# Optimization experiments

Measured on AMD Instinct MI355X. Metric: run time of the kernel, lower is better.

The kernel has to match this reference:

```python
import jax, jax.numpy as jnp
from jax import lax
import numpy as np

B, R, NOBJ, SIZE = 16, 64, 32, 64  # batch, rels/image, objs/image, map size


def setup_inputs() -> dict:
    key = jax.random.key(0)
    ks = jax.random.split(key, 8)
    # boxes as (x1, y1, x2, y2) in an arbitrary image coordinate frame
    xy1 = jax.random.uniform(ks[0], (B, NOBJ, 2), dtype=jnp.float32) * 80.0
    wh = jax.random.uniform(ks[1], (B, NOBJ, 2), dtype=jnp.float32) * 40.0 + 2.0
    bboxes = jnp.concatenate([xy1, xy1 + wh], axis=-1)  # [B, NOBJ, 4]
    num_obj = jnp.full((B,), NOBJ, dtype=jnp.int32)
    num_relation = jnp.full((B,), R, dtype=jnp.int32)  # constant -> static tot_num_rels
    object_pairs = jax.random.randint(ks[2], (B, R, 2), 0, NOBJ)
    conv1_w = jax.random.normal(ks[3], (64, 2, 5, 5), dtype=jnp.float32) * 0.1
    conv1_b = jnp.zeros((64,), dtype=jnp.float32)
    conv2_w = jax.random.normal(ks[4], (32, 64, 5, 5), dtype=jnp.float32) * 0.05
    conv2_b = jnp.zeros((32,), dtype=jnp.float32)
    fc_w = jax.random.normal(ks[5], (512, 32), dtype=jnp.float32) * 0.1
    fc_b = jnp.zeros((512,), dtype=jnp.float32)
    return dict(bboxes=bboxes, num_obj=num_obj, num_relation=num_relation,
                object_pairs=object_pairs, conv1_w=conv1_w, conv1_b=conv1_b,
                conv2_w=conv2_w, conv2_b=conv2_b, fc_w=fc_w, fc_b=fc_b)


def _sp_maps(bboxes, object_pairs):
    # Vectorized replacement of the per-relation python loop + get_sp:
    # both boxes of a pair are rescaled into the 64x64 frame of their union
    # box and rasterized as binary masks (iCAN-style 2-channel spatial config).
    Bc, Rc, _ = object_pairs.shape
    pairs = object_pairs.reshape(-1, 2)                      # [T, 2]
    b_idx = jnp.repeat(jnp.arange(Bc), Rc)                   # [T]
    b0 = bboxes[b_idx, pairs[:, 0]]                          # [T, 4]
    b1 = bboxes[b_idx, pairs[:, 1]]                          # [T, 4]
    ux1 = jnp.minimum(b0[:, 0], b1[:, 0])
    uy1 = jnp.minimum(b0[:, 1], b1[:, 1])
    ux2 = jnp.maximum(b0[:, 2], b1[:, 2])
    uy2 = jnp.maximum(b0[:, 3], b1[:, 3])
    uw = jnp.maximum(ux2 - ux1, 1e-6)
    uh = jnp.maximum(uy2 - uy1, 1e-6)

    def scale(b):  # union-normalized box in [0, SIZE] grid coords
        return jnp.stack([(b[:, 0] - ux1) / uw * SIZE,
                          (b[:, 1] - uy1) / uh * SIZE,
                          (b[:, 2] - ux1) / uw * SIZE,
                          (b[:, 3] - uy1) / uh * SIZE], axis=-1)

    coords = jnp.arange(SIZE, dtype=jnp.float32) + 0.5
    gx = coords[None, None, :]   # [1, 1, SIZE]
    gy = coords[None, :, None]   # [1, SIZE, 1]

    def rasterize(sb):  # sb: [T, 4] -> [T, SIZE, SIZE]
        x1 = sb[:, 0, None, None]; y1 = sb[:, 1, None, None]
        x2 = sb[:, 2, None, None]; y2 = sb[:, 3, None, None]
        return ((gx >= x1) & (gx <= x2) & (gy >= y1) & (gy <= y2)).astype(jnp.float32)

    return jnp.stack([rasterize(scale(b0)), rasterize(scale(b1))], axis=1)  # [T,2,64,64]


def _conv(x, w, b):
    y = lax.conv_general_dilated(x, w, window_strides=(1, 1), padding='VALID',
                                 dimension_numbers=('NCHW', 'OIHW', 'NCHW'))
    return y + b[None, :, None, None]


def _maxpool2(x):
    return lax.reduce_window(x, -jnp.inf, lax.max, (1, 1, 2, 2), (1, 1, 2, 2), 'VALID')


def reference(bboxes, num_obj, num_relation, object_pairs,
              conv1_w, conv1_b, conv2_w, conv2_b, fc_w, fc_b):
    sp = _sp_maps(bboxes, object_pairs)        # [T, 2, 64, 64]
    x = _maxpool2(_conv(sp, conv1_w, conv1_b)) # [T, 64, 30, 30]
    x = _maxpool2(_conv(x, conv2_w, conv2_b))  # [T, 32, 13, 13]
    x = jnp.mean(x, axis=(2, 3))               # AvgPool((13,13)) -> [T, 32]
    return jax.nn.relu(x @ fc_w.T + fc_b)      # [T, 512]
```

## Files before the change

kernel.cpp:

```cpp
#include <hip/hip_runtime.h>
#include <stdint.h>

typedef unsigned long long u64;
typedef short v8s __attribute__((ext_vector_type(8)));
typedef float v4f __attribute__((ext_vector_type(4)));

__device__ __forceinline__ unsigned short f2bf_rne(float f) {
  union { float f; unsigned u; } c; c.f = f;
  unsigned u = c.u;
  u += 0x7fffu + ((u >> 16) & 1u);
  return (unsigned short)(u >> 16);
}

__global__ __launch_bounds__(256) void prepack_w2(
    const float* __restrict__ w2, unsigned short* __restrict__ Wr) {
  int idx = blockIdx.x * 256 + threadIdx.x;
  if (idx >= 32 * 1600) return;
  int c = idx / 1600, rem = idx - c * 1600;
  int h = rem / 800, r2 = rem - h * 800;
  int tap = r2 >> 5, chh = r2 & 31;
  Wr[h * 25600 + c * 800 + r2] = f2bf_rne(w2[(c * 64 + h * 32 + chh) * 25 + tap]);
}

__global__ __launch_bounds__(512, 4) void fused_kernel(
    const float* __restrict__ bboxes,
    const int*   __restrict__ pairs,
    const float* __restrict__ w1,
    const float* __restrict__ b1,
    const unsigned short* __restrict__ Wr,
    const float* __restrict__ b2,
    const float* __restrict__ fcw,
    const float* __restrict__ fcb,
    float* __restrict__ out)
{
  extern __shared__ char smem[];
  unsigned short* Xs = (unsigned short*)smem;
  float* P8      = (float*)(smem + 61200);
  float* Cout    = (float*)smem;
  float* partial = (float*)(smem + 61200);
  float* fs      = (float*)(smem + 61200 + 1024);

  const int n = blockIdx.x, t = threadIdx.x;
  const int lane = t & 63, wv = t >> 6;
  const int q = lane >> 4, ln = lane & 15;

  const int bb = n >> 6, rr_ = n & 63;
  const int p0 = pairs[(bb * 64 + rr_) * 2 + 0];
  const int p1 = pairs[(bb * 64 + rr_) * 2 + 1];
  const float* A  = bboxes + (bb * 32 + p0) * 4;
  const float* Bq = bboxes + (bb * 32 + p1) * 4;
  const float ax1 = A[0],  ay1 = A[1],  ax2 = A[2],  ay2 = A[3];
  const float cx1 = Bq[0], cy1 = Bq[1], cx2 = Bq[2], cy2 = Bq[3];
  const float ux1 = fminf(ax1, cx1), uy1 = fminf(ay1, cy1);
  const float ux2 = fmaxf(ax2, cx2), uy2 = fmaxf(ay2, cy2);
  const float uw = fmaxf(ux2 - ux1, 1e-6f), uh = fmaxf(uy2 - uy1, 1e-6f);
  const float g = (float)lane + 0.5f;
  u64 ixs[2], iys[2];
  {
    float X1 = (ax1 - ux1) / uw * 64.f, X2 = (ax2 - ux1) / uw * 64.f;
    float Y1 = (ay1 - uy1) / uh * 64.f, Y2 = (ay2 - uy1) / uh * 64.f;
    ixs[0] = __ballot(g >= X1 && g <= X2);
    iys[0] = __ballot(g >= Y1 && g <= Y2);
  }
  {
    float X1 = (cx1 - ux1) / uw * 64.f, X2 = (cx2 - ux1) / uw * 64.f;
    float Y1 = (cy1 - uy1) / uh * 64.f, Y2 = (cy2 - uy1) / uh * 64.f;
    ixs[1] = __ballot(g >= X1 && g <= X2);
    iys[1] = __ballot(g >= Y1 && g <= Y2);
  }

  v4f acc[6][2];
  int pclamp[6], baseB[6];
  int cnt = 0;
  #pragma unroll
  for (int it = 0; it < 6; it++) {
    int nt = wv + it * 8;
    if (nt < 43) {
      int p = nt * 16 + ln; if (p > 675) p = 675;
      pclamp[it] = p;
      int y = p / 26, x = p - y * 26;
      baseB[it] = (y * 30 + x) * 68 + q * 16;
      cnt = it + 1;
    } else { pclamp[it] = 0; baseB[it] = 0; }
    acc[it][0] = (v4f)0.f; acc[it][1] = (v4f)0.f;
  }

  for (int h = 0; h < 2; h++) {
    for (int c8 = 0; c8 < 4; c8++) {
      const int cbase = h * 32 + c8 * 8;
      for (int e = t; e < 960; e += 512) {
        int cidx = e / 120, rem = e - cidx * 120;
        int ch = rem / 60, x = rem - ch * 60;
        unsigned bits = (unsigned)(ixs[ch] >> x) & 31u;
        const float* wr = w1 + (cbase + cidx) * 50 + ch * 25;
        float* Pp = P8 + cidx * 610 + ch * 305 + x;
        float p = 0.f;
        #pragma unroll
        for (int i = 0; i < 5; i++) {
          float rcv = 0.f;
          #pragma unroll
          for (int j = 0; j < 5; j++)
            rcv += ((bits >> j) & 1u) ? wr[i * 5 + j] : 0.f;
          p += rcv;
          Pp[i * 61] = p;
        }
      }
      __syncthreads();
      float b1v[8];
      #pragma unroll
      for (int i = 0; i < 8; i++) b1v[i] = b1[cbase + i];
      for (int pix = t; pix < 900; pix += 512) {
        int qy = pix / 30, qx = pix - qy * 30;
        int x0f = 2 * qx;
        int zo[2][2], ao[2][2]; bool sub[2][2], act[2][2], same[2];
        #pragma unroll
        for (int ch = 0; ch < 2; ch++) {
          unsigned m0 = (unsigned)(iys[ch] >> (2 * qy)) & 31u;
          unsigned m1 = (unsigned)(iys[ch] >> (2 * qy + 1)) & 31u;
          act[ch][0] = m0 != 0; act[ch][1] = m1 != 0;
          zo[ch][0] = (31 - __clz((int)(m0 | 1u))) * 61;
          zo[ch][1] = (31 - __clz((int)(m1 | 1u))) * 61;
          int a0 = __ffs((int)m0) - 1, a1 = __ffs((int)m1) - 1;
          sub[ch][0] = a0 > 0; ao[ch][0] = (a0 > 0 ? a0 - 1 : 0) * 61;
          sub[ch][1] = a1 > 0; ao[ch][1] = (a1 > 0 ? a1 - 1 : 0) * 61;
          same[ch] = (m0 == m1);
        }
        unsigned outs[4];
        #pragma unroll
        for (int cidx = 0; cidx < 8; cidx++) {
          float v0 = 0.f, v1 = 0.f, w0 = 0.f, w1 = 0.f;
          #pragma unroll
          for (int ch = 0; ch < 2; ch++) {
            const float* Pc = P8 + cidx * 610 + ch * 305 + x0f;
            float z0 = Pc[zo[ch][0]], z1 = Pc[zo[ch][0] + 1];
            float pa0 = Pc[ao[ch][0]], pa1 = Pc[ao[ch][0] + 1];
            float d0 = z0 - (sub[ch][0] ? pa0 : 0.f);
            float d1 = z1 - (sub[ch][0] ? pa1 : 0.f);
            d0 = act[ch][0] ? d0 : 0.f;
            d1 = act[ch][0] ? d1 : 0.f;
            v0 += d0; v1 += d1;
            if (same[ch]) { w0 += d0; w1 += d1; }
            else {
              float e0 = Pc[zo[ch][1]], e1 = Pc[zo[ch][1] + 1];
              float f0 = Pc[ao[ch][1]], f1 = Pc[ao[ch][1] + 1];
              float g0 = e0 - (sub[ch][1] ? f0 : 0.f);
              float g1 = e1 - (sub[ch][1] ? f1 : 0.f);
              w0 += act[ch][1] ? g0 : 0.f;
              w1 += act[ch][1] ? g1 : 0.f;
            }
          }
          float mx = fmaxf(fmaxf(v0, v1), fmaxf(w0, w1)) + b1v[cidx];
          unsigned bf = (unsigned)f2bf_rne(mx);
          if ((cidx & 1) == 0) outs[cidx >> 1] = bf;
          else                 outs[cidx >> 1] |= bf << 16;
        }
        unsigned* xw = (unsigned*)(Xs + pix * 34 + c8 * 8);
        xw[0] = outs[0]; xw[1] = outs[1]; xw[2] = outs[2]; xw[3] = outs[3];
      }
      __syncthreads();
    }

    const unsigned short* pA0 = Wr + h * 25600 + ln * 800 + q * 8;
    const unsigned short* pA1 = pA0 + 16 * 800;
    for (int i = 0; i < 5; i++) {
      const int rowoff = i * 2040;
      #pragma unroll
      for (int jt = 0; jt < 5; jt++) {
        const int s = i * 5 + jt;
        v8s a0 = *(const v8s*)(pA0 + s * 32);
        v8s a1 = *(const v8s*)(pA1 + s * 32);
        const int off = rowoff + jt * 68;
        #pragma unroll
        for (int it = 0; it < 6; it++) {
          if (it < cnt) {
            const unsigned* bp = (const unsigned*)(smem + (baseB[it] + off));
            uint4 bv; bv.x = bp[0]; bv.y = bp[1]; bv.z = bp[2]; bv.w = bp[3];
            v8s b = __builtin_bit_cast(v8s, bv);
            acc[it][0] = __builtin_amdgcn_mfma_f32_16x16x32_bf16(a0, b, acc[it][0], 0, 0, 0);
            acc[it][1] = __builtin_amdgcn_mfma_f32_16x16x32_bf16(a1, b, acc[it][1], 0, 0, 0);
          }
        }
      }
    }
  }

  #pragma unroll
  for (int mt = 0; mt < 2; mt++) {
    __syncthreads();
    #pragma unroll
    for (int it = 0; it < 6; it++) {
      if (it < cnt) {
        #pragma unroll
        for (int r = 0; r < 4; r++)
          Cout[(q * 4 + r) * 677 + pclamp[it]] = acc[it][mt][r];
      }
    }
    __syncthreads();
    if (t < 208) {
      int c = t & 15, py = t >> 4;
      const float* r0 = Cout + c * 677 + (2 * py) * 26;
      const float* r1 = r0 + 26;
      float s = 0.f;
      #pragma unroll
      for (int px = 0; px < 13; px++) {
        float m0 = fmaxf(r0[2 * px], r0[2 * px + 1]);
        float m1 = fmaxf(r1[2 * px], r1[2 * px + 1]);
        s += fmaxf(m0, m1);
      }
      partial[t] = s;
    }
    __syncthreads();
    if (t < 16) {
      float s = 0.f;
      #pragma unroll
      for (int k = 0; k < 13; k++) s += partial[k * 16 + t];
      fs[mt * 16 + t] = s * (1.f / 169.f) + b2[mt * 16 + t];
    }
  }
  __syncthreads();

  {
    const float* wrow = fcw + t * 32;
    float d = 0.f;
    #pragma unroll
    for (int k = 0; k < 32; k++) d += wrow[k] * fs[k];
    out[(u64)n * 512 + t] = fmaxf(d + fcb[t], 0.f);
  }
}

extern "C" void kernel_launch(void* const* d_in, const int* in_sizes, int n_in,
                              void* d_out, int out_size, void* d_ws, size_t ws_size,
                              hipStream_t stream) {
  const float* bboxes = (const float*)d_in[0];
  const int*   pairs  = (const int*)  d_in[3];
  const float* w1     = (const float*)d_in[4];
  const float* b1     = (const float*)d_in[5];
  const float* w2     = (const float*)d_in[6];
  const float* b2     = (const float*)d_in[7];
  const float* fcw    = (const float*)d_in[8];
  const float* fcb    = (const float*)d_in[9];
  float* out = (float*)d_out;

  unsigned short* Wr = (unsigned short*)d_ws;

  prepack_w2<<<(32 * 1600 + 255) / 256, 256, 0, stream>>>(w2, Wr);
  fused_kernel<<<1024, 512, 80720, stream>>>(bboxes, pairs, w1, b1, Wr, b2,
                                             fcw, fcb, out);
}
```

Before: 257.6 us.

## Deduplicate identical conv1 pooled rows via row-signature grouping

Wavefront 0 computes a per-pooled-row signature from the y-masks of both boxes and groups identical rows. Conv1+pool is then evaluated once per unique row and scattered to every row that shares it. Channels are processed in groups of 4 instead of 8, and the bf16 activation row pitch changes from 68 to 72 bytes so the MFMA B-operand loads become 8-byte aligned pairs. The shared-memory footprint drops as well. The cost is an extra sync and the dedup logic, plus a serial scatter loop whose length depends on how many rows repeat, and twice as many channel-group iterations and barriers.

```diff
diff --git a/kernel.cpp b/kernel.cpp
--- a/kernel.cpp
+++ b/kernel.cpp
@@ -34,11 +34,13 @@
     float* __restrict__ out)
 {
   extern __shared__ char smem[];
-  unsigned short* Xs = (unsigned short*)smem;
-  float* P8      = (float*)(smem + 61200);
-  float* Cout    = (float*)smem;
-  float* partial = (float*)(smem + 61200);
-  float* fs      = (float*)(smem + 61200 + 1024);
+  float* P4       = (float*)(smem + 64800);
+  unsigned* repmaskL = (unsigned*)(smem + 74560);
+  unsigned* repsigL  = (unsigned*)(smem + 74680);
+  int* nrepL         = (int*)(smem + 74800);
+  float* partial     = (float*)(smem + 74816);
+  float* fs          = (float*)(smem + 75648);
+  float* Cout        = (float*)smem;
 
   const int n = blockIdx.x, t = threadIdx.x;
   const int lane = t & 63, wv = t >> 6;
@@ -69,6 +71,32 @@
     iys[1] = __ballot(g >= Y1 && g <= Y2);
   }
 
+  if (wv == 0) {
+    unsigned sig;
+    if (lane < 30) {
+      unsigned m00 = (unsigned)(iys[0] >> (2 * lane))     & 31u;
+      unsigned m01 = (unsigned)(iys[0] >> (2 * lane + 1)) & 31u;
+      unsigned m10 = (unsigned)(iys[1] >> (2 * lane))     & 31u;
+      unsigned m11 = (unsigned)(iys[1] >> (2 * lane + 1)) & 31u;
+      sig = m00 | (m01 << 5) | (m10 << 10) | (m11 << 15);
+    } else sig = 0x80000000u | (unsigned)lane;
+    int myrep = lane;
+    for (int k = 0; k < 30; k++) {
+      unsigned sk = (unsigned)__shfl((int)sig, k);
+      if (sk == sig && k < myrep) myrep = k;
+    }
+    u64 repsb = __ballot(myrep == lane && lane < 30);
+    if (lane < 30) repmaskL[lane] = 0u;
+    if (lane < 30) {
+      int j = __popcll(repsb & ((1ull << myrep) - 1));
+      atomicOr(&repmaskL[j], 1u << lane);
+      if (myrep == lane) repsigL[j] = sig;
+    }
+    if (lane == 0) nrepL[0] = (int)__popcll(repsb);
+  }
+  __syncthreads();
+  const int nrep = nrepL[0];
+
   v4f acc[6][2];
   int pclamp[6], baseB[6];
   int cnt = 0;
@@ -79,21 +107,21 @@
       int p = nt * 16 + ln; if (p > 675) p = 675;
       pclamp[it] = p;
       int y = p / 26, x = p - y * 26;
-      baseB[it] = (y * 30 + x) * 68 + q * 16;
+      baseB[it] = (y * 30 + x) * 72 + q * 16;
       cnt = it + 1;
     } else { pclamp[it] = 0; baseB[it] = 0; }
     acc[it][0] = (v4f)0.f; acc[it][1] = (v4f)0.f;
   }
 
   for (int h = 0; h < 2; h++) {
-    for (int c8 = 0; c8 < 4; c8++) {
-      const int cbase = h * 32 + c8 * 8;
-      for (int e = t; e < 960; e += 512) {
+    for (int c4 = 0; c4 < 8; c4++) {
+      const int cbase = h * 32 + c4 * 4;
+      for (int e = t; e < 480; e += 512) {
         int cidx = e / 120, rem = e - cidx * 120;
         int ch = rem / 60, x = rem - ch * 60;
         unsigned bits = (unsigned)(ixs[ch] >> x) & 31u;
         const float* wr = w1 + (cbase + cidx) * 50 + ch * 25;
-        float* Pp = P8 + cidx * 610 + ch * 305 + x;
+        float* Pp = P4 + (cidx * 2 + ch) * 305 + x;
         float p = 0.f;
         #pragma unroll
         for (int i = 0; i < 5; i++) {
@@ -106,56 +134,38 @@
         }
       }
       __syncthreads();
-      float b1v[8];
-      #pragma unroll
-      for (int i = 0; i < 8; i++) b1v[i] = b1[cbase + i];
-      for (int pix = t; pix < 900; pix += 512) {
-        int qy = pix / 30, qx = pix - qy * 30;
-        int x0f = 2 * qx;
-        int zo[2][2], ao[2][2]; bool sub[2][2], act[2][2], same[2];
+      for (int e = t; e < nrep * 120; e += 512) {
+        int r = e / 120, rem = e - r * 120;
+        int cidx = rem / 30, qx = rem - cidx * 30;
+        unsigned sig = repsigL[r];
+        float v00 = 0.f, v01 = 0.f, v10 = 0.f, v11 = 0.f;
         #pragma unroll
         for (int ch = 0; ch < 2; ch++) {
-          unsigned m0 = (unsigned)(iys[ch] >> (2 * qy)) & 31u;
-          unsigned m1 = (unsigned)(iys[ch] >> (2 * qy + 1)) & 31u;
-          act[ch][0] = m0 != 0; act[ch][1] = m1 != 0;
-          zo[ch][0] = (31 - __clz((int)(m0 | 1u))) * 61;
-          zo[ch][1] = (31 - __clz((int)(m1 | 1u))) * 61;
-          int a0 = __ffs((int)m0) - 1, a1 = __ffs((int)m1) - 1;
-          sub[ch][0] = a0 > 0; ao[ch][0] = (a0 > 0 ? a0 - 1 : 0) * 61;
-          sub[ch][1] = a1 > 0; ao[ch][1] = (a1 > 0 ? a1 - 1 : 0) * 61;
-          same[ch] = (m0 == m1);
-        }
-        unsigned outs[4];
-        #pragma unroll
-        for (int cidx = 0; cidx < 8; cidx++) {
-          float v0 = 0.f, v1 = 0.f, w0 = 0.f, w1 = 0.f;
+          const float* Pc = P4 + (cidx * 2 + ch) * 305 + 2 * qx;
           #pragma unroll
-          for (int ch = 0; ch < 2; ch++) {
-            const float* Pc = P8 + cidx * 610 + ch * 305 + x0f;
-            float z0 = Pc[zo[ch][0]], z1 = Pc[zo[ch][0] + 1];
-            float pa0 = Pc[ao[ch][0]], pa1 = Pc[ao[ch][0] + 1];
-            float d0 = z0 - (sub[ch][0] ? pa0 : 0.f);
-            float d1 = z1 - (sub[ch][0] ? pa1 : 0.f);
-            d0 = act[ch][0] ? d0 : 0.f;
-            d1 = act[ch][0] ? d1 : 0.f;
-            v0 += d0; v1 += d1;
-            if (same[ch]) { w0 += d0; w1 += d1; }
-            else {
-              float e0 = Pc[zo[ch][1]], e1 = Pc[zo[ch][1] + 1];
-              float f0 = Pc[ao[ch][1]], f1 = Pc[ao[ch][1] + 1];
-              float g0 = e0 - (sub[ch][1] ? f0 : 0.f);
-              float g1 = e1 - (sub[ch][1] ? f1 : 0.f);
-              w0 += act[ch][1] ? g0 : 0.f;
-              w1 += act[ch][1] ? g1 : 0.f;
-            }
+          for (int dy = 0; dy < 2; dy++) {
+            unsigned m = (sig >> (ch * 10 + dy * 5)) & 31u;
+            bool act = m != 0;
+            int zrow = 31 - __clz((int)(m | 1u));
+            int a = __ffs((int)m) - 1;
+            bool sub = a > 0;
+            int arow = sub ? a - 1 : 0;
+            float z0 = Pc[zrow * 61], z1 = Pc[zrow * 61 + 1];
+            float a0v = Pc[arow * 61], a1v = Pc[arow * 61 + 1];
+            float d0 = act ? (z0 - (sub ? a0v : 0.f)) : 0.f;
+            float d1 = act ? (z1 - (sub ? a1v : 0.f)) : 0.f;
+            if (dy == 0) { v00 += d0; v01 += d1; }
+            else         { v10 += d0; v11 += d1; }
           }
-          float mx = fmaxf(fmaxf(v0, v1), fmaxf(w0, w1)) + b1v[cidx];
-          unsigned bf = (unsigned)f2bf_rne(mx);
-          if ((cidx & 1) == 0) outs[cidx >> 1] = bf;
-          else                 outs[cidx >> 1] |= bf << 16;
-        }
-        unsigned* xw = (unsigned*)(Xs + pix * 34 + c8 * 8);
-        xw[0] = outs[0]; xw[1] = outs[1]; xw[2] = outs[2]; xw[3] = outs[3];
+        }
+        float mx = fmaxf(fmaxf(v00, v01), fmaxf(v10, v11)) + b1[cbase + cidx];
+        unsigned short val = f2bf_rne(mx);
+        int base = qx * 72 + (c4 * 4 + cidx) * 2;
+        unsigned m = repmaskL[r];
+        while (m) {
+          int qy = __ffs((int)m) - 1; m &= m - 1;
+          *(unsigned short*)(smem + qy * 2160 + base) = val;
+        }
       }
       __syncthreads();
     }
@@ -163,18 +173,19 @@
     const unsigned short* pA0 = Wr + h * 25600 + ln * 800 + q * 8;
     const unsigned short* pA1 = pA0 + 16 * 800;
     for (int i = 0; i < 5; i++) {
-      const int rowoff = i * 2040;
+      const int rowoff = i * 2160;
       #pragma unroll
       for (int jt = 0; jt < 5; jt++) {
         const int s = i * 5 + jt;
         v8s a0 = *(const v8s*)(pA0 + s * 32);
         v8s a1 = *(const v8s*)(pA1 + s * 32);
-        const int off = rowoff + jt * 68;
+        const int off = rowoff + jt * 72;
         #pragma unroll
         for (int it = 0; it < 6; it++) {
           if (it < cnt) {
-            const unsigned* bp = (const unsigned*)(smem + (baseB[it] + off));
-            uint4 bv; bv.x = bp[0]; bv.y = bp[1]; bv.z = bp[2]; bv.w = bp[3];
+            uint2 lo = *(const uint2*)(smem + (baseB[it] + off));
+            uint2 hi = *(const uint2*)(smem + (baseB[it] + off + 8));
+            uint4 bv; bv.x = lo.x; bv.y = lo.y; bv.z = hi.x; bv.w = hi.y;
             v8s b = __builtin_bit_cast(v8s, bv);
             acc[it][0] = __builtin_amdgcn_mfma_f32_16x16x32_bf16(a0, b, acc[it][0], 0, 0, 0);
             acc[it][1] = __builtin_amdgcn_mfma_f32_16x16x32_bf16(a1, b, acc[it][1], 0, 0, 0);
@@ -244,6 +255,6 @@
   unsigned short* Wr = (unsigned short*)d_ws;
 
   prepack_w2<<<(32 * 1600 + 255) / 256, 256, 0, stream>>>(w2, Wr);
-  fused_kernel<<<1024, 512, 80720, stream>>>(bboxes, pairs, w1, b1, Wr, b2,
+  fused_kernel<<<1024, 512, 75776, stream>>>(bboxes, pairs, w1, b1, Wr, b2,
                                              fcw, fcb, out);
 }
```

Result: slower. 426.8 us (+65.7%).

## Restructure conv1 stage into 4-channel chunks with hoisted row indices and padded layouts

Applied to the files above, without the earlier changes.

Conv1 channels are now processed in chunks of 4 instead of 8. The prefix-sum table gains a leading zero row so the subtract and active branches disappear. The per-pixel row-mask offsets are computed once, hoisted out of the channel loop. The X tile row stride goes from 68 to 72 bytes, which allows 8-byte aligned stores and uint2 loads for the MFMA B operand, and shared memory shrinks slightly. In exchange there are twice as many barrier-separated chunk iterations, half the threads sit idle in the prefix phase, and more registers are held across the loop.

```diff
diff --git a/kernel.cpp b/kernel.cpp
--- a/kernel.cpp
+++ b/kernel.cpp
@@ -34,11 +34,10 @@
     float* __restrict__ out)
 {
   extern __shared__ char smem[];
-  unsigned short* Xs = (unsigned short*)smem;
-  float* P8      = (float*)(smem + 61200);
+  float* P4      = (float*)(smem + 64800);
+  float* partial = (float*)(smem + 76320);
+  float* fs      = (float*)(smem + 77152);
   float* Cout    = (float*)smem;
-  float* partial = (float*)(smem + 61200);
-  float* fs      = (float*)(smem + 61200 + 1024);
 
   const int n = blockIdx.x, t = threadIdx.x;
   const int lane = t & 63, wv = t >> 6;
@@ -69,6 +68,29 @@
     iys[1] = __ballot(g >= Y1 && g <= Y2);
   }
 
+  int qx2_[2], xsb_[2];
+  int zo_[2][2][2], ao_[2][2][2];
+  bool same_[2][2];
+  #pragma unroll
+  for (int pp = 0; pp < 2; pp++) {
+    int pix = t + pp * 512;
+    bool vld = pix < 900;
+    int qy = vld ? pix / 30 : 0;
+    int qx = vld ? pix - qy * 30 : 0;
+    qx2_[pp] = 2 * qx;
+    xsb_[pp] = pix * 72;
+    #pragma unroll
+    for (int ch = 0; ch < 2; ch++) {
+      unsigned m0 = (unsigned)(iys[ch] >> (2 * qy))     & 31u;
+      unsigned m1 = (unsigned)(iys[ch] >> (2 * qy + 1)) & 31u;
+      zo_[pp][ch][0] = (m0 ? 32 - __clz((int)m0) : 0) * 60;
+      ao_[pp][ch][0] = (m0 ? __ffs((int)m0) - 1  : 0) * 60;
+      zo_[pp][ch][1] = (m1 ? 32 - __clz((int)m1) : 0) * 60;
+      ao_[pp][ch][1] = (m1 ? __ffs((int)m1) - 1  : 0) * 60;
+      same_[pp][ch] = (m0 == m1);
+    }
+  }
+
   v4f acc[6][2];
   int pclamp[6], baseB[6];
   int cnt = 0;
@@ -79,22 +101,23 @@
       int p = nt * 16 + ln; if (p > 675) p = 675;
       pclamp[it] = p;
       int y = p / 26, x = p - y * 26;
-      baseB[it] = (y * 30 + x) * 68 + q * 16;
+      baseB[it] = (y * 30 + x) * 72 + q * 16;
       cnt = it + 1;
     } else { pclamp[it] = 0; baseB[it] = 0; }
     acc[it][0] = (v4f)0.f; acc[it][1] = (v4f)0.f;
   }
 
   for (int h = 0; h < 2; h++) {
-    for (int c8 = 0; c8 < 4; c8++) {
-      const int cbase = h * 32 + c8 * 8;
-      for (int e = t; e < 960; e += 512) {
+    for (int c4 = 0; c4 < 8; c4++) {
+      const int cbase = h * 32 + c4 * 4;
+      for (int e = t; e < 480; e += 512) {
         int cidx = e / 120, rem = e - cidx * 120;
         int ch = rem / 60, x = rem - ch * 60;
         unsigned bits = (unsigned)(ixs[ch] >> x) & 31u;
         const float* wr = w1 + (cbase + cidx) * 50 + ch * 25;
-        float* Pp = P8 + cidx * 610 + ch * 305 + x;
+        float* Pp = P4 + (cidx * 2 + ch) * 360 + x;
         float p = 0.f;
+        Pp[0] = 0.f;
         #pragma unroll
         for (int i = 0; i < 5; i++) {
           float rcv = 0.f;
@@ -102,60 +125,43 @@
           for (int j = 0; j < 5; j++)
             rcv += ((bits >> j) & 1u) ? wr[i * 5 + j] : 0.f;
           p += rcv;
-          Pp[i * 61] = p;
+          Pp[(i + 1) * 60] = p;
         }
       }
       __syncthreads();
-      float b1v[8];
-      #pragma unroll
-      for (int i = 0; i < 8; i++) b1v[i] = b1[cbase + i];
-      for (int pix = t; pix < 900; pix += 512) {
-        int qy = pix / 30, qx = pix - qy * 30;
-        int x0f = 2 * qx;
-        int zo[2][2], ao[2][2]; bool sub[2][2], act[2][2], same[2];
-        #pragma unroll
-        for (int ch = 0; ch < 2; ch++) {
-          unsigned m0 = (unsigned)(iys[ch] >> (2 * qy)) & 31u;
-          unsigned m1 = (unsigned)(iys[ch] >> (2 * qy + 1)) & 31u;
-          act[ch][0] = m0 != 0; act[ch][1] = m1 != 0;
-          zo[ch][0] = (31 - __clz((int)(m0 | 1u))) * 61;
-          zo[ch][1] = (31 - __clz((int)(m1 | 1u))) * 61;
-          int a0 = __ffs((int)m0) - 1, a1 = __ffs((int)m1) - 1;
-          sub[ch][0] = a0 > 0; ao[ch][0] = (a0 > 0 ? a0 - 1 : 0) * 61;
-          sub[ch][1] = a1 > 0; ao[ch][1] = (a1 > 0 ? a1 - 1 : 0) * 61;
-          same[ch] = (m0 == m1);
+      float b1v[4];
+      #pragma unroll
+      for (int i = 0; i < 4; i++) b1v[i] = b1[cbase + i];
+      #pragma unroll
+      for (int pp = 0; pp < 2; pp++) {
+        int pix = t + pp * 512;
+        if (pix < 900) {
+          unsigned outs[2];
+          #pragma unroll
+          for (int cidx = 0; cidx < 4; cidx++) {
+            float v00 = 0.f, v01 = 0.f, v10 = 0.f, v11 = 0.f;
+            #pragma unroll
+            for (int ch = 0; ch < 2; ch++) {
+              const float* Pc = P4 + (cidx * 2 + ch) * 360 + qx2_[pp];
+              float2 z0 = *(const float2*)(Pc + zo_[pp][ch][0]);
+              float2 a0 = *(const float2*)(Pc + ao_[pp][ch][0]);
+              float d0 = z0.x - a0.x, d1 = z0.y - a0.y;
+              v00 += d0; v01 += d1;
+              if (same_[pp][ch]) { v10 += d0; v11 += d1; }
+              else {
+                float2 z1 = *(const float2*)(Pc + zo_[pp][ch][1]);
+                float2 a1 = *(const float2*)(Pc + ao_[pp][ch][1]);
+                v10 += z1.x - a1.x; v11 += z1.y - a1.y;
+              }
+            }
+            float mx = fmaxf(fmaxf(v00, v01), fmaxf(v10, v11)) + b1v[cidx];
+            unsigned bf = (unsigned)f2bf_rne(mx);
+            if ((cidx & 1) == 0) outs[cidx >> 1] = bf;
+            else                 outs[cidx >> 1] |= bf << 16;
+          }
+          uint2 pk; pk.x = outs[0]; pk.y = outs[1];
+          *(uint2*)(smem + xsb_[pp] + c4 * 8) = pk;
         }
-        unsigned outs[4];
-        #pragma unroll
-        for (int cidx = 0; cidx < 8; cidx++) {
-          float v0 = 0.f, v1 = 0.f, w0 = 0.f, w1 = 0.f;
-          #pragma unroll
-          for (int ch = 0; ch < 2; ch++) {
-            const float* Pc = P8 + cidx * 610 + ch * 305 + x0f;
-            float z0 = Pc[zo[ch][0]], z1 = Pc[zo[ch][0] + 1];
-            float pa0 = Pc[ao[ch][0]], pa1 = Pc[ao[ch][0] + 1];
-            float d0 = z0 - (sub[ch][0] ? pa0 : 0.f);
-            float d1 = z1 - (sub[ch][0] ? pa1 : 0.f);
-            d0 = act[ch][0] ? d0 : 0.f;
-            d1 = act[ch][0] ? d1 : 0.f;
-            v0 += d0; v1 += d1;
-            if (same[ch]) { w0 += d0; w1 += d1; }
-            else {
-              float e0 = Pc[zo[ch][1]], e1 = Pc[zo[ch][1] + 1];
-              float f0 = Pc[ao[ch][1]], f1 = Pc[ao[ch][1] + 1];
-              float g0 = e0 - (sub[ch][1] ? f0 : 0.f);
-              float g1 = e1 - (sub[ch][1] ? f1 : 0.f);
-              w0 += act[ch][1] ? g0 : 0.f;
-              w1 += act[ch][1] ? g1 : 0.f;
-            }
-          }
-          float mx = fmaxf(fmaxf(v0, v1), fmaxf(w0, w1)) + b1v[cidx];
-          unsigned bf = (unsigned)f2bf_rne(mx);
-          if ((cidx & 1) == 0) outs[cidx >> 1] = bf;
-          else                 outs[cidx >> 1] |= bf << 16;
-        }
-        unsigned* xw = (unsigned*)(Xs + pix * 34 + c8 * 8);
-        xw[0] = outs[0]; xw[1] = outs[1]; xw[2] = outs[2]; xw[3] = outs[3];
       }
       __syncthreads();
     }
@@ -163,18 +169,19 @@
     const unsigned short* pA0 = Wr + h * 25600 + ln * 800 + q * 8;
     const unsigned short* pA1 = pA0 + 16 * 800;
     for (int i = 0; i < 5; i++) {
-      const int rowoff = i * 2040;
+      const int rowoff = i * 2160;
       #pragma unroll
       for (int jt = 0; jt < 5; jt++) {
         const int s = i * 5 + jt;
         v8s a0 = *(const v8s*)(pA0 + s * 32);
         v8s a1 = *(const v8s*)(pA1 + s * 32);
-        const int off = rowoff + jt * 68;
+        const int off = rowoff + jt * 72;
         #pragma unroll
         for (int it = 0; it < 6; it++) {
           if (it < cnt) {
-            const unsigned* bp = (const unsigned*)(smem + (baseB[it] + off));
-            uint4 bv; bv.x = bp[0]; bv.y = bp[1]; bv.z = bp[2]; bv.w = bp[3];
+            uint2 lo = *(const uint2*)(smem + (baseB[it] + off));
+            uint2 hi = *(const uint2*)(smem + (baseB[it] + off + 8));
+            uint4 bv; bv.x = lo.x; bv.y = lo.y; bv.z = hi.x; bv.w = hi.y;
             v8s b = __builtin_bit_cast(v8s, bv);
             acc[it][0] = __builtin_amdgcn_mfma_f32_16x16x32_bf16(a0, b, acc[it][0], 0, 0, 0);
             acc[it][1] = __builtin_amdgcn_mfma_f32_16x16x32_bf16(a1, b, acc[it][1], 0, 0, 0);
@@ -244,6 +251,6 @@
   unsigned short* Wr = (unsigned short*)d_ws;
 
   prepack_w2<<<(32 * 1600 + 255) / 256, 256, 0, stream>>>(w2, Wr);
-  fused_kernel<<<1024, 512, 80720, stream>>>(bboxes, pairs, w1, b1, Wr, b2,
+  fused_kernel<<<1024, 512, 77280, stream>>>(bboxes, pairs, w1, b1, Wr, b2,
                                              fcw, fcb, out);
 }
```

Result: slower. 395.6 us (+53.5%).
